# Kernel optimization log

Hardware: AMD Instinct MI355X
Metric: run time of the kernel (lower is better)

## Reference

```python
import jax, jax.numpy as jnp
import numpy as np
from jax.scipy.linalg import expm

DIM = 128
BF = 2          # branching_factor
H = 8           # num_heads
MAX_DEPTH = 12
PAD = BF + 1    # padding value used by pad_sequence in the torch module
N = 256         # number of positions


def setup_inputs() -> dict:
    key = jax.random.key(0)
    k1, k2 = jax.random.split(key)
    # raw _primitives parameter (the torch init applies softmax+cumsum to rand;
    # any values work for the math -- only the skew-hermitian part matters)
    prim = jax.random.uniform(k1, (BF * H + 1, DIM, DIM), dtype=jnp.float32)
    positions = jax.random.randint(k2, (N,), 0, BF ** MAX_DEPTH)  # node indices, >= 0
    return {"primitives_param": prim, "positions": positions}


def _path_words(positions):
    """Vectorized equivalent of create_paths + pad_sequence.

    For node index n the branch path is built by walking up the tree:
    branch = (n-1) % BF, parent = (n-1) // BF. Digits come out leaf->root,
    so we reverse the valid prefix and right-pad with PAD to MAX_DEPTH.
    """
    d = positions.astype(jnp.int32)
    digs = []
    for _ in range(MAX_DEPTH):
        valid = d > 0
        digs.append(jnp.where(valid, (d - 1) % BF, PAD))
        d = jnp.where(valid, (d - 1) // BF, 0)
    R = jnp.stack(digs, axis=1)            # (N, 12) leaf->root digits
    depth = jnp.sum(R != PAD, axis=1)       # path length per token
    idx = depth[:, None] - 1 - jnp.arange(MAX_DEPTH)[None, :]
    pw = jnp.take_along_axis(R, jnp.clip(idx, 0, MAX_DEPTH - 1), axis=1)
    pw = jnp.where(idx >= 0, pw, PAD)       # (N, 12) root->leaf, PAD-padded
    return pw, depth


def reference(primitives_param, positions):
    pw, depth = _path_words(positions)

    # ---- steps matrix (tree distance), mirrors the no_grad block ----
    pm = pw != PAD                                        # (N, 12)
    mask = pm[:, None, :] & pm[None, :, :]                # (N, N, 12)
    eq = pw[:, None, :] == pw[None, :, :]
    common = jnp.cumprod(eq.astype(jnp.int32), axis=-1).astype(bool) & mask
    cpl = common.sum(-1)                                  # common prefix length
    steps = depth[:, None] + depth[None, :] - 2 * cpl     # (N, N) int

    # ---- unitary primitives: expm of the skew(-hermitian, real) part ----
    skew = primitives_param - jnp.swapaxes(primitives_param, -1, -2)
    prims = expm(skew)                                    # (BF*H+1, DIM, DIM)
    sos = prims[-1]
    P = prims[:-1].reshape(BF, H, DIM, DIM)

    n_tok = pw.shape[0]
    maps = jnp.broadcast_to(jnp.eye(DIM, dtype=prims.dtype)[None, None],
                            (n_tok, H, DIM, DIM))
    sos_ptr = pw[:, 0] == -1                              # never true for pos>=0, kept for fidelity
    maps = jnp.where(sos_ptr[:, None, None, None], sos[None, None], maps)

    # fused gather-indexed scan over tree depth: instead of BF masked matmuls
    # per depth, gather each token's branch primitive and do one batched matmul.
    for d in range(MAX_DEPTH):
        sel = pw[:, d]                                    # (N,) in {0..BF-1} or PAD
        Pk = P[jnp.clip(sel, 0, BF - 1)]                  # (N, H, DIM, DIM)
        new = jnp.einsum('nhij,nhjk->nhik', maps, Pk)
        maps = jnp.where((sel < BF)[:, None, None, None], new, maps)

    return maps, steps
```

## Files before the change

### kernel.cpp

```cpp
#include <hip/hip_runtime.h>

typedef unsigned short ushort_t;
typedef unsigned int uint_t;
typedef __attribute__((ext_vector_type(8))) short bf16x8;
typedef __attribute__((ext_vector_type(4))) float f32x4;

#define NMAT 16
#define MSZ 16384
#define NTAB 30

__device__ __forceinline__ ushort_t f32_bf16(float f) {
  uint_t u = __builtin_bit_cast(uint_t, f);
  u += 0x7FFFu + ((u >> 16) & 1u);
  return (ushort_t)(u >> 16);
}

__device__ __forceinline__ float bf16_f32(ushort_t b) {
  uint_t u = ((uint_t)b) << 16;
  return __builtin_bit_cast(float, u);
}

__device__ __forceinline__ int swz(int r, int k) {
  return r * 128 + (((k >> 3) ^ (r & 7)) << 3) + (k & 7);
}

__device__ __forceinline__ int tab_off(int L) {
  return (L == 1) ? 0 : (L == 2) ? 2 : (L == 3) ? 6 : 14;
}

__device__ __forceinline__ void mm_frag(const ushort_t* U, const ushort_t* V,
                                        int r0, int c0, int quad, int l16,
                                        f32x4 (&acc)[4][4]) {
#pragma unroll
  for (int rt = 0; rt < 4; rt++)
#pragma unroll
    for (int ct = 0; ct < 4; ct++) {
      f32x4 z = {0.f, 0.f, 0.f, 0.f};
      acc[rt][ct] = z;
    }
#pragma unroll
  for (int kt = 0; kt < 4; kt++) {
    int k = kt * 32 + quad * 8;
    bf16x8 a[4], b[4];
#pragma unroll
    for (int rt = 0; rt < 4; rt++) a[rt] = *(const bf16x8*)(&U[swz(r0 + rt * 16 + l16, k)]);
#pragma unroll
    for (int ct = 0; ct < 4; ct++) b[ct] = *(const bf16x8*)(&V[swz(c0 + ct * 16 + l16, k)]);
#pragma unroll
    for (int rt = 0; rt < 4; rt++)
#pragma unroll
      for (int ct = 0; ct < 4; ct++)
        acc[rt][ct] = __builtin_amdgcn_mfma_f32_16x16x32_bf16(a[rt], b[ct], acc[rt][ct], 0, 0, 0);
  }
}

__device__ __forceinline__ void store_T(ushort_t* dst, const f32x4 (&acc)[4][4],
                                        int r0, int c0, int quad, int l16,
                                        float scale, float cdiag) {
#pragma unroll
  for (int rt = 0; rt < 4; rt++)
#pragma unroll
    for (int ct = 0; ct < 4; ct++) {
      int dr = r0 + rt * 16 + quad * 4, dc = c0 + ct * 16 + l16;
      float v[4];
#pragma unroll
      for (int i = 0; i < 4; i++) {
        v[i] = scale * acc[rt][ct][i];
        if (dr + i == dc) v[i] += cdiag;
      }
      uint2 pk;
      pk.x = (uint_t)f32_bf16(v[0]) | ((uint_t)f32_bf16(v[1]) << 16);
      pk.y = (uint_t)f32_bf16(v[2]) | ((uint_t)f32_bf16(v[3]) << 16);
      *(uint2*)(&dst[swz(dc, dr)]) = pk;
    }
}

__device__ __forceinline__ void set_ident(ushort_t* dst, int t, float c) {
  ushort_t cb = f32_bf16(c);
  for (int i = 0; i < 64; i++) {
    int e = i * 256 + t;
    int r = e >> 7, k = e & 127;
    dst[swz(r, k)] = (r == k) ? cb : (ushort_t)0;
  }
}

__global__ __launch_bounds__(256, 1) void expm1_kernel(const float* __restrict__ prim,
                                                       ushort_t* __restrict__ wsCS) {
  __shared__ ushort_t __align__(16) bufA[MSZ];
  __shared__ ushort_t __align__(16) bufB[MSZ];
  int kmat = blockIdx.x >> 1, which = blockIdx.x & 1;
  int t = threadIdx.x, wave = t >> 6, lane = t & 63;
  int quad = lane >> 4, l16 = lane & 15;
  int r0 = (wave >> 1) * 64, c0 = (wave & 1) * 64;
  const float* p = prim + kmat * MSZ;

  for (int i = 0; i < 64; i++) {
    int e = i * 256 + t;
    int r = e >> 7, c = e & 127;
    bufA[swz(r, c)] = f32_bf16((p[r * 128 + c] - p[c * 128 + r]) * 0.125f);
  }
  __syncthreads();

  f32x4 acc[4][4];
  mm_frag(bufA, bufA, r0, c0, quad, l16, acc);
  __syncthreads();
  store_T(bufB, acc, r0, c0, quad, l16, -1.f, 0.f);
  __syncthreads();

  uint2 yv[4][4];
#pragma unroll
  for (int rt = 0; rt < 4; rt++)
#pragma unroll
    for (int ct = 0; ct < 4; ct++) {
      int dr = r0 + rt * 16 + quad * 4, dc = c0 + ct * 16 + l16;
      yv[rt][ct] = *(const uint2*)(&bufB[swz(dc, dr)]);
    }

  mm_frag(bufB, bufB, r0, c0, quad, l16, acc);
  __syncthreads();
  store_T(bufB, acc, r0, c0, quad, l16, 1.f, 0.f);

  float coef[9];
  if (which == 0) {
    coef[0] = 1.f; coef[1] = 1.f / 2; coef[2] = 1.f / 24; coef[3] = 1.f / 720;
    coef[4] = 1.f / 40320; coef[5] = 1.f / 3628800.f; coef[6] = 1.f / 479001600.f;
    coef[7] = 1.f / 87178291200.f; coef[8] = 1.f / 20922789888000.f;
  } else {
    coef[0] = 1.f; coef[1] = 1.f / 6; coef[2] = 1.f / 120; coef[3] = 1.f / 5040;
    coef[4] = 1.f / 362880.f; coef[5] = 1.f / 39916800.f; coef[6] = 1.f / 6227020800.f;
    coef[7] = 1.f / 1307674368000.f; coef[8] = 1.f / 355687428096000.f;
  }

  set_ident(bufA, t, coef[8]);
  __syncthreads();

#pragma unroll
  for (int k = 3; k >= 0; k--) {
    mm_frag(bufB, bufA, r0, c0, quad, l16, acc);
    __syncthreads();
    float cd = coef[2 * k], cy = coef[2 * k + 1];
#pragma unroll
    for (int rt = 0; rt < 4; rt++)
#pragma unroll
      for (int ct = 0; ct < 4; ct++) {
        int dr = r0 + rt * 16 + quad * 4, dc = c0 + ct * 16 + l16;
        uint2 yp = yv[rt][ct];
        float y[4] = {bf16_f32((ushort_t)(yp.x & 0xffff)), bf16_f32((ushort_t)(yp.x >> 16)),
                      bf16_f32((ushort_t)(yp.y & 0xffff)), bf16_f32((ushort_t)(yp.y >> 16))};
        float v[4];
#pragma unroll
        for (int i = 0; i < 4; i++) {
          v[i] = acc[rt][ct][i] + cy * y[i];
          if (dr + i == dc) v[i] += cd;
        }
        uint2 pk;
        pk.x = (uint_t)f32_bf16(v[0]) | ((uint_t)f32_bf16(v[1]) << 16);
        pk.y = (uint_t)f32_bf16(v[2]) | ((uint_t)f32_bf16(v[3]) << 16);
        *(uint2*)(&bufA[swz(dc, dr)]) = pk;
      }
    __syncthreads();
  }
  ushort_t* dst = wsCS + (size_t)(which * NMAT + kmat) * MSZ;
  for (int i = 0; i < 8; i++) {
    int e = (i * 256 + t) * 8;
    int r = e >> 7, k = e & 127;
    *(uint4*)(dst + e) = *(const uint4*)(&bufA[swz(r, k)]);
  }
}

__global__ __launch_bounds__(256, 1) void expm2_kernel(
    const float* __restrict__ prim, const ushort_t* __restrict__ wsCS,
    ushort_t* __restrict__ TN, ushort_t* __restrict__ TT) {
  __shared__ ushort_t __align__(16) bufA[MSZ];
  __shared__ ushort_t __align__(16) bufB[MSZ];
  int kmat = blockIdx.x;
  int t = threadIdx.x, wave = t >> 6, lane = t & 63;
  int quad = lane >> 4, l16 = lane & 15;
  int r0 = (wave >> 1) * 64, c0 = (wave & 1) * 64;
  const float* p = prim + kmat * MSZ;
  const ushort_t* Cg = wsCS + (size_t)kmat * MSZ;
  const ushort_t* Sg = wsCS + (size_t)(NMAT + kmat) * MSZ;

  for (int i = 0; i < 64; i++) {
    int e = i * 256 + t;
    int r = e >> 7, c = e & 127;
    bufA[swz(r, c)] = f32_bf16((p[r * 128 + c] - p[c * 128 + r]) * 0.125f);
  }
  for (int i = 0; i < 8; i++) {
    int e = (i * 256 + t) * 8;
    int r = e >> 7, k = e & 127;
    *(uint4*)(&bufB[swz(r, k)]) = *(const uint4*)(Sg + e);
  }
  __syncthreads();

  f32x4 acc[4][4];
  mm_frag(bufA, bufB, r0, c0, quad, l16, acc);
  __syncthreads();
#pragma unroll
  for (int rt = 0; rt < 4; rt++)
#pragma unroll
    for (int ct = 0; ct < 4; ct++) {
      int dr = r0 + rt * 16 + quad * 4, dc = c0 + ct * 16 + l16;
      uint2 cp = *(const uint2*)(Cg + dc * 128 + dr);
      float cf[4] = {bf16_f32((ushort_t)(cp.x & 0xffff)), bf16_f32((ushort_t)(cp.x >> 16)),
                     bf16_f32((ushort_t)(cp.y & 0xffff)), bf16_f32((ushort_t)(cp.y >> 16))};
      uint2 en, et;
      en.x = (uint_t)f32_bf16(cf[0] - acc[rt][ct][0]) | ((uint_t)f32_bf16(cf[1] - acc[rt][ct][1]) << 16);
      en.y = (uint_t)f32_bf16(cf[2] - acc[rt][ct][2]) | ((uint_t)f32_bf16(cf[3] - acc[rt][ct][3]) << 16);
      et.x = (uint_t)f32_bf16(cf[0] + acc[rt][ct][0]) | ((uint_t)f32_bf16(cf[1] + acc[rt][ct][1]) << 16);
      et.y = (uint_t)f32_bf16(cf[2] + acc[rt][ct][2]) | ((uint_t)f32_bf16(cf[3] + acc[rt][ct][3]) << 16);
      *(uint2*)(&bufA[swz(dc, dr)]) = en;
      *(uint2*)(&bufB[swz(dc, dr)]) = et;
    }
  __syncthreads();

#pragma unroll 1
  for (int sq = 0; sq < 3; sq++) {
    mm_frag(bufA, bufB, r0, c0, quad, l16, acc);
    __syncthreads();
#pragma unroll
    for (int rt = 0; rt < 4; rt++)
#pragma unroll
      for (int ct = 0; ct < 4; ct++) {
        int dr = r0 + rt * 16 + quad * 4, dc = c0 + ct * 16 + l16;
        uint2 pk;
        pk.x = (uint_t)f32_bf16(acc[rt][ct][0]) | ((uint_t)f32_bf16(acc[rt][ct][1]) << 16);
        pk.y = (uint_t)f32_bf16(acc[rt][ct][2]) | ((uint_t)f32_bf16(acc[rt][ct][3]) << 16);
        *(uint2*)(&bufB[swz(dc, dr)]) = pk;
#pragma unroll
        for (int i = 0; i < 4; i++) bufA[swz(dr + i, dc)] = f32_bf16(acc[rt][ct][i]);
      }
    __syncthreads();
  }
  for (int i = 0; i < 8; i++) {
    int e = (i * 256 + t) * 8;
    int r = e >> 7, k = e & 127;
    *(uint4*)(TN + (size_t)kmat * MSZ + e) = *(const uint4*)(&bufA[swz(r, k)]);
    *(uint4*)(TT + (size_t)kmat * MSZ + e) = *(const uint4*)(&bufB[swz(r, k)]);
  }
}

__global__ __launch_bounds__(256) void table_kernel(ushort_t* __restrict__ TN,
                                                    ushort_t* __restrict__ TT, int mode) {
  int bx = blockIdx.x;
  int eA, eB, eO, h;
  if (mode == 0) {
    int c = bx >> 3; h = bx & 7;
    eA = c >> 1; eB = c & 1; eO = 2 + c;
  } else {
    if (bx < 64) {
      int c = bx >> 3; h = bx & 7;
      eA = 2 + (c >> 1); eB = c & 1; eO = 6 + c;
    } else {
      int c = (bx - 64) >> 3; h = (bx - 64) & 7;
      eA = 2 + (c >> 2); eB = 2 + (c & 3); eO = 14 + c;
    }
  }
  int t = threadIdx.x, wave = t >> 6, lane = t & 63;
  int quad = lane >> 4, l16 = lane & 15;
  int r0 = (wave >> 1) * 64, c0 = (wave & 1) * 64;
  const ushort_t* A = TN + ((size_t)eA * 8 + h) * MSZ;
  const ushort_t* B = TT + ((size_t)eB * 8 + h) * MSZ;
  ushort_t* oN = TN + ((size_t)eO * 8 + h) * MSZ;
  ushort_t* oT = TT + ((size_t)eO * 8 + h) * MSZ;

  bf16x8 a[4][4], b[4][4];
#pragma unroll
  for (int kt = 0; kt < 4; kt++) {
#pragma unroll
    for (int rt = 0; rt < 4; rt++)
      a[kt][rt] = *(const bf16x8*)(A + (r0 + rt * 16 + l16) * 128 + kt * 32 + quad * 8);
#pragma unroll
    for (int ct = 0; ct < 4; ct++)
      b[kt][ct] = *(const bf16x8*)(B + (c0 + ct * 16 + l16) * 128 + kt * 32 + quad * 8);
  }
  f32x4 acc[4][4];
#pragma unroll
  for (int rt = 0; rt < 4; rt++)
#pragma unroll
    for (int ct = 0; ct < 4; ct++) {
      f32x4 z = {0.f, 0.f, 0.f, 0.f};
      acc[rt][ct] = z;
    }
#pragma unroll
  for (int kt = 0; kt < 4; kt++)
#pragma unroll
    for (int rt = 0; rt < 4; rt++)
#pragma unroll
      for (int ct = 0; ct < 4; ct++)
        acc[rt][ct] = __builtin_amdgcn_mfma_f32_16x16x32_bf16(a[kt][rt], b[kt][ct], acc[rt][ct], 0, 0, 0);
#pragma unroll
  for (int rt = 0; rt < 4; rt++)
#pragma unroll
    for (int ct = 0; ct < 4; ct++) {
      int dr = r0 + rt * 16 + quad * 4, dc = c0 + ct * 16 + l16;
      uint2 pk;
      pk.x = (uint_t)f32_bf16(acc[rt][ct][0]) | ((uint_t)f32_bf16(acc[rt][ct][1]) << 16);
      pk.y = (uint_t)f32_bf16(acc[rt][ct][2]) | ((uint_t)f32_bf16(acc[rt][ct][3]) << 16);
      *(uint2*)(oT + dc * 128 + dr) = pk;
#pragma unroll
      for (int i = 0; i < 4; i++) oN[(dr + i) * 128 + dc] = f32_bf16(acc[rt][ct][i]);
    }
}

__global__ void steps_kernel(const int* __restrict__ pos, float* __restrict__ os, int N) {
  int i = blockIdx.x, j = threadIdx.x;
  int mi = pos[i] + 1, mj = pos[j] + 1;
  int di = 31 - __builtin_clz((unsigned)mi);
  int dj = 31 - __builtin_clz((unsigned)mj);
  int tt = di < dj ? di : dj;
  unsigned x = (unsigned)((mi >> (di - tt)) ^ (mj >> (dj - tt)));
  int cpl = tt - (x ? (32 - __builtin_clz(x)) : 0);
  os[i * N + j] = (float)(di + dj - 2 * cpl);
}

__global__ __launch_bounds__(256, 2) void maps_kernel(
    const ushort_t* __restrict__ TN, const ushort_t* __restrict__ TT,
    const int* __restrict__ positions, float* __restrict__ out) {
  __shared__ ushort_t __align__(16) Mb[2][MSZ];
  int bx = blockIdx.x;
  int n = bx >> 3, h = bx & 7;
  int t = threadIdx.x, wave = t >> 6, lane = t & 63;
  int quad = lane >> 4, l16 = lane & 15;
  int m = positions[n] + 1;
  int depth = 31 - __builtin_clz((unsigned)m);
  float* ob = out + (size_t)(n * 8 + h) * MSZ;

  if (depth == 0) {
    for (int i = 0; i < 64; i++) {
      int e = i * 256 + t;
      int r = e >> 7, k = e & 127;
      ob[e] = (r == k) ? 1.0f : 0.0f;
    }
    return;
  }
  if (depth <= 4) {
    int c = m & ((1 << depth) - 1);
    const ushort_t* src = TN + ((size_t)(tab_off(depth) + c) * 8 + h) * MSZ;
    for (int i = 0; i < 8; i++) {
      int e = (i * 256 + t) * 8;
      bf16x8 v = *(const bf16x8*)(src + e);
      f32x4 lo = {bf16_f32((ushort_t)v[0]), bf16_f32((ushort_t)v[1]),
                  bf16_f32((ushort_t)v[2]), bf16_f32((ushort_t)v[3])};
      f32x4 hi = {bf16_f32((ushort_t)v[4]), bf16_f32((ushort_t)v[5]),
                  bf16_f32((ushort_t)v[6]), bf16_f32((ushort_t)v[7])};
      *(f32x4*)(ob + e) = lo;
      *(f32x4*)(ob + e + 4) = hi;
    }
    return;
  }

  int K = (depth + 3) >> 2;
  int L0 = depth - 4 * (K - 1);
  int c0v = (m >> (depth - L0)) & ((1 << L0) - 1);
  const ushort_t* src0 = TN + ((size_t)(tab_off(L0) + c0v) * 8 + h) * MSZ;
  bool two = (K == 3);
  int c1 = (m >> (4 * (K - 2))) & 15;
  int c2 = m & 15;
  const ushort_t* Ap1 = TT + ((size_t)(14 + c1) * 8 + h) * MSZ;
  const ushort_t* Ap2 = TT + ((size_t)(14 + c2) * 8 + h) * MSZ;

  int r0 = (wave >> 1) * 64, c0 = (wave & 1) * 64;
#pragma unroll
  for (int i = 0; i < 8; i++) {
    int e = (i * 256 + t) * 8;
    int r = e >> 7, k = e & 127;
    *(uint4*)(&Mb[0][swz(r, k)]) = *(const uint4*)(src0 + e);
  }
  bf16x8 a1[4][4];
#pragma unroll
  for (int kt = 0; kt < 4; kt++)
#pragma unroll
    for (int rt = 0; rt < 4; rt++)
      a1[kt][rt] = *(const bf16x8*)(Ap1 + (r0 + rt * 16 + l16) * 128 + kt * 32 + quad * 8);
  __syncthreads();

  f32x4 acc[4][4];
#pragma unroll
  for (int rt = 0; rt < 4; rt++)
#pragma unroll
    for (int ct = 0; ct < 4; ct++) {
      f32x4 z = {0.f, 0.f, 0.f, 0.f};
      acc[rt][ct] = z;
    }
#pragma unroll
  for (int kt = 0; kt < 4; kt++) {
    int k = kt * 32 + quad * 8;
    bf16x8 b[4];
#pragma unroll
    for (int ct = 0; ct < 4; ct++) b[ct] = *(const bf16x8*)(&Mb[0][swz(c0 + ct * 16 + l16, k)]);
#pragma unroll
    for (int rt = 0; rt < 4; rt++)
#pragma unroll
      for (int ct = 0; ct < 4; ct++)
        acc[rt][ct] = __builtin_amdgcn_mfma_f32_16x16x32_bf16(a1[kt][rt], b[ct], acc[rt][ct], 0, 0, 0);
  }

  if (two) {
    bf16x8 a2[4][4];
#pragma unroll
    for (int kt = 0; kt < 4; kt++)
#pragma unroll
      for (int rt = 0; rt < 4; rt++)
        a2[kt][rt] = *(const bf16x8*)(Ap2 + (r0 + rt * 16 + l16) * 128 + kt * 32 + quad * 8);
#pragma unroll
    for (int rt = 0; rt < 4; rt++)
#pragma unroll
      for (int ct = 0; ct < 4; ct++) {
        int dr = r0 + rt * 16 + quad * 4;
        int dc = c0 + ct * 16 + l16;
        uint2 pk;
        pk.x = (uint_t)f32_bf16(acc[rt][ct][0]) | ((uint_t)f32_bf16(acc[rt][ct][1]) << 16);
        pk.y = (uint_t)f32_bf16(acc[rt][ct][2]) | ((uint_t)f32_bf16(acc[rt][ct][3]) << 16);
        *(uint2*)(&Mb[1][swz(dc, dr)]) = pk;
      }
    __syncthreads();

#pragma unroll
    for (int rt = 0; rt < 4; rt++)
#pragma unroll
      for (int ct = 0; ct < 4; ct++) {
        f32x4 z = {0.f, 0.f, 0.f, 0.f};
        acc[rt][ct] = z;
      }
#pragma unroll
    for (int kt = 0; kt < 4; kt++) {
      int k = kt * 32 + quad * 8;
      bf16x8 b[4];
#pragma unroll
      for (int ct = 0; ct < 4; ct++) b[ct] = *(const bf16x8*)(&Mb[1][swz(c0 + ct * 16 + l16, k)]);
#pragma unroll
      for (int rt = 0; rt < 4; rt++)
#pragma unroll
        for (int ct = 0; ct < 4; ct++)
          acc[rt][ct] = __builtin_amdgcn_mfma_f32_16x16x32_bf16(a2[kt][rt], b[ct], acc[rt][ct], 0, 0, 0);
    }
  }

#pragma unroll
  for (int rt = 0; rt < 4; rt++)
#pragma unroll
    for (int ct = 0; ct < 4; ct++) {
      int dr = r0 + rt * 16 + quad * 4;
      int dc = c0 + ct * 16 + l16;
      *(f32x4*)(ob + dc * 128 + dr) = acc[rt][ct];
    }
}

extern "C" void kernel_launch(void* const* d_in, const int* in_sizes, int n_in,
                              void* d_out, int out_size, void* d_ws, size_t ws_size,
                              hipStream_t stream) {
  const float* prim = (const float*)d_in[0];
  const int* positions = (const int*)d_in[1];
  int N = in_sizes[1];
  float* out = (float*)d_out;

  ushort_t* wsCS = (ushort_t*)d_ws;
  ushort_t* TN = wsCS + (size_t)2 * NMAT * MSZ;
  ushort_t* TT = TN + (size_t)NTAB * 8 * MSZ;

  steps_kernel<<<N, N, 0, stream>>>(positions, out + (size_t)N * 8 * MSZ, N);
  expm1_kernel<<<2 * NMAT, 256, 0, stream>>>(prim, wsCS);
  expm2_kernel<<<NMAT, 256, 0, stream>>>(prim, wsCS, TN, TT);
  table_kernel<<<32, 256, 0, stream>>>(TN, TT, 0);
  table_kernel<<<192, 256, 0, stream>>>(TN, TT, 1);
  maps_kernel<<<N * 8, 256, 0, stream>>>(TN, TT, positions, out);
}
```

Baseline: 221.4 us.

## Fuse steps into expm1, merge table kernels, stage transpose through LDS

Folds the steps-matrix computation into extra blocks of the first expm kernel, which removes one launch. The two table-building launches become a single launch in which depth-3 and depth-4 entries are recomputed from the base entries through chained in-block matmuls in LDS, removing the launch dependency between them. The skew-part construction now stages the fp32 matrix in swizzled shared memory so the transposed read no longer hits global memory uncoalesced. The cost is redundant matmul work in the table blocks and an added bf16 rounding for intermediate products.

Result: slower. 231.8 us (+4.7%).

```diff
diff --git a/kernel.cpp b/kernel.cpp
--- a/kernel.cpp
+++ b/kernel.cpp
@@ -46,6 +46,58 @@
     for (int rt = 0; rt < 4; rt++) a[rt] = *(const bf16x8*)(&U[swz(r0 + rt * 16 + l16, k)]);
 #pragma unroll
     for (int ct = 0; ct < 4; ct++) b[ct] = *(const bf16x8*)(&V[swz(c0 + ct * 16 + l16, k)]);
+#pragma unroll
+    for (int rt = 0; rt < 4; rt++)
+#pragma unroll
+      for (int ct = 0; ct < 4; ct++)
+        acc[rt][ct] = __builtin_amdgcn_mfma_f32_16x16x32_bf16(a[rt], b[ct], acc[rt][ct], 0, 0, 0);
+  }
+}
+
+__device__ __forceinline__ void mm_gg(const ushort_t* gU, const ushort_t* gV,
+                                      int r0, int c0, int quad, int l16,
+                                      f32x4 (&acc)[4][4]) {
+#pragma unroll
+  for (int rt = 0; rt < 4; rt++)
+#pragma unroll
+    for (int ct = 0; ct < 4; ct++) {
+      f32x4 z = {0.f, 0.f, 0.f, 0.f};
+      acc[rt][ct] = z;
+    }
+#pragma unroll
+  for (int kt = 0; kt < 4; kt++) {
+    int k = kt * 32 + quad * 8;
+    bf16x8 a[4], b[4];
+#pragma unroll
+    for (int rt = 0; rt < 4; rt++) a[rt] = *(const bf16x8*)(gU + (r0 + rt * 16 + l16) * 128 + k);
+#pragma unroll
+    for (int ct = 0; ct < 4; ct++) b[ct] = *(const bf16x8*)(gV + (c0 + ct * 16 + l16) * 128 + k);
+#pragma unroll
+    for (int rt = 0; rt < 4; rt++)
+#pragma unroll
+      for (int ct = 0; ct < 4; ct++)
+        acc[rt][ct] = __builtin_amdgcn_mfma_f32_16x16x32_bf16(a[rt], b[ct], acc[rt][ct], 0, 0, 0);
+  }
+}
+
+__device__ __forceinline__ void mm_lg(const ushort_t* lU, const ushort_t* gV,
+                                      int r0, int c0, int quad, int l16,
+                                      f32x4 (&acc)[4][4]) {
+#pragma unroll
+  for (int rt = 0; rt < 4; rt++)
+#pragma unroll
+    for (int ct = 0; ct < 4; ct++) {
+      f32x4 z = {0.f, 0.f, 0.f, 0.f};
+      acc[rt][ct] = z;
+    }
+#pragma unroll
+  for (int kt = 0; kt < 4; kt++) {
+    int k = kt * 32 + quad * 8;
+    bf16x8 a[4], b[4];
+#pragma unroll
+    for (int rt = 0; rt < 4; rt++) a[rt] = *(const bf16x8*)(&lU[swz(r0 + rt * 16 + l16, k)]);
+#pragma unroll
+    for (int ct = 0; ct < 4; ct++) b[ct] = *(const bf16x8*)(gV + (c0 + ct * 16 + l16) * 128 + k);
 #pragma unroll
     for (int rt = 0; rt < 4; rt++)
 #pragma unroll
@@ -84,12 +136,30 @@
   }
 }
 
-__global__ __launch_bounds__(256, 1) void expm1_kernel(const float* __restrict__ prim,
-                                                       ushort_t* __restrict__ wsCS) {
-  __shared__ ushort_t __align__(16) bufA[MSZ];
-  __shared__ ushort_t __align__(16) bufB[MSZ];
-  int kmat = blockIdx.x >> 1, which = blockIdx.x & 1;
-  int t = threadIdx.x, wave = t >> 6, lane = t & 63;
+__global__ __launch_bounds__(256, 1) void expm1_kernel(
+    const float* __restrict__ prim, ushort_t* __restrict__ wsCS,
+    const int* __restrict__ pos, float* __restrict__ os, int N) {
+  int bx = blockIdx.x;
+  int t = threadIdx.x;
+  if (bx >= 32) {
+    int i = bx - 32, j = t;
+    int mi = pos[i] + 1, mj = pos[j] + 1;
+    int di = 31 - __builtin_clz((unsigned)mi);
+    int dj = 31 - __builtin_clz((unsigned)mj);
+    int tt = di < dj ? di : dj;
+    unsigned x = (unsigned)((mi >> (di - tt)) ^ (mj >> (dj - tt)));
+    int cpl = tt - (x ? (32 - __builtin_clz(x)) : 0);
+    os[i * N + j] = (float)(di + dj - 2 * cpl);
+    return;
+  }
+
+  __shared__ ushort_t __align__(16) smem[2 * MSZ];
+  ushort_t* bufA = smem;
+  ushort_t* bufB = smem + MSZ;
+  float* pf = (float*)smem;
+
+  int kmat = bx >> 1, which = bx & 1;
+  int wave = t >> 6, lane = t & 63;
   int quad = lane >> 4, l16 = lane & 15;
   int r0 = (wave >> 1) * 64, c0 = (wave & 1) * 64;
   const float* p = prim + kmat * MSZ;
@@ -97,7 +167,24 @@
   for (int i = 0; i < 64; i++) {
     int e = i * 256 + t;
     int r = e >> 7, c = e & 127;
-    bufA[swz(r, c)] = f32_bf16((p[r * 128 + c] - p[c * 128 + r]) * 0.125f);
+    pf[r * 128 + (c ^ (r & 31))] = p[e];
+  }
+  __syncthreads();
+  ushort_t xr[64];
+#pragma unroll
+  for (int i = 0; i < 64; i++) {
+    int e = i * 256 + t;
+    int r = e >> 7, c = e & 127;
+    float a = pf[r * 128 + (c ^ (r & 31))];
+    float b = pf[c * 128 + (r ^ (c & 31))];
+    xr[i] = f32_bf16((a - b) * 0.125f);
+  }
+  __syncthreads();
+#pragma unroll
+  for (int i = 0; i < 64; i++) {
+    int e = i * 256 + t;
+    int r = e >> 7, c = e & 127;
+    bufA[swz(r, c)] = xr[i];
   }
   __syncthreads();
 
@@ -171,8 +258,10 @@
 __global__ __launch_bounds__(256, 1) void expm2_kernel(
     const float* __restrict__ prim, const ushort_t* __restrict__ wsCS,
     ushort_t* __restrict__ TN, ushort_t* __restrict__ TT) {
-  __shared__ ushort_t __align__(16) bufA[MSZ];
-  __shared__ ushort_t __align__(16) bufB[MSZ];
+  __shared__ ushort_t __align__(16) smem[2 * MSZ];
+  ushort_t* bufA = smem;
+  ushort_t* bufB = smem + MSZ;
+  float* pf = (float*)smem;
   int kmat = blockIdx.x;
   int t = threadIdx.x, wave = t >> 6, lane = t & 63;
   int quad = lane >> 4, l16 = lane & 15;
@@ -184,7 +273,24 @@
   for (int i = 0; i < 64; i++) {
     int e = i * 256 + t;
     int r = e >> 7, c = e & 127;
-    bufA[swz(r, c)] = f32_bf16((p[r * 128 + c] - p[c * 128 + r]) * 0.125f);
+    pf[r * 128 + (c ^ (r & 31))] = p[e];
+  }
+  __syncthreads();
+  ushort_t xr[64];
+#pragma unroll
+  for (int i = 0; i < 64; i++) {
+    int e = i * 256 + t;
+    int r = e >> 7, c = e & 127;
+    float a = pf[r * 128 + (c ^ (r & 31))];
+    float b = pf[c * 128 + (r ^ (c & 31))];
+    xr[i] = f32_bf16((a - b) * 0.125f);
+  }
+  __syncthreads();
+#pragma unroll
+  for (int i = 0; i < 64; i++) {
+    int e = i * 256 + t;
+    int r = e >> 7, c = e & 127;
+    bufA[swz(r, c)] = xr[i];
   }
   for (int i = 0; i < 8; i++) {
     int e = (i * 256 + t) * 8;
@@ -241,54 +347,45 @@
 }
 
 __global__ __launch_bounds__(256) void table_kernel(ushort_t* __restrict__ TN,
-                                                    ushort_t* __restrict__ TT, int mode) {
+                                                    ushort_t* __restrict__ TT) {
+  __shared__ ushort_t __align__(16) LA[MSZ];
+  __shared__ ushort_t __align__(16) LB[MSZ];
   int bx = blockIdx.x;
-  int eA, eB, eO, h;
-  if (mode == 0) {
-    int c = bx >> 3; h = bx & 7;
-    eA = c >> 1; eB = c & 1; eO = 2 + c;
-  } else {
-    if (bx < 64) {
-      int c = bx >> 3; h = bx & 7;
-      eA = 2 + (c >> 1); eB = c & 1; eO = 6 + c;
-    } else {
-      int c = (bx - 64) >> 3; h = (bx - 64) & 7;
-      eA = 2 + (c >> 2); eB = 2 + (c & 3); eO = 14 + c;
-    }
-  }
+  int idx = bx >> 3, h = bx & 7;
   int t = threadIdx.x, wave = t >> 6, lane = t & 63;
   int quad = lane >> 4, l16 = lane & 15;
   int r0 = (wave >> 1) * 64, c0 = (wave & 1) * 64;
-  const ushort_t* A = TN + ((size_t)eA * 8 + h) * MSZ;
-  const ushort_t* B = TT + ((size_t)eB * 8 + h) * MSZ;
+  f32x4 acc[4][4];
+  int eO;
+  (void)t;
+
+  if (idx < 4) {
+    int c = idx; eO = 2 + c;
+    mm_gg(TN + ((size_t)(c >> 1) * 8 + h) * MSZ,
+          TT + ((size_t)(c & 1) * 8 + h) * MSZ, r0, c0, quad, l16, acc);
+  } else if (idx < 12) {
+    int c = idx - 4; eO = 6 + c;
+    int a = c >> 2, b = (c >> 1) & 1, last = c & 1;
+    mm_gg(TT + ((size_t)b * 8 + h) * MSZ,
+          TN + ((size_t)a * 8 + h) * MSZ, r0, c0, quad, l16, acc);
+    store_T(LA, acc, r0, c0, quad, l16, 1.f, 0.f);
+    __syncthreads();
+    mm_lg(LA, TT + ((size_t)last * 8 + h) * MSZ, r0, c0, quad, l16, acc);
+  } else {
+    int c = idx - 12; eO = 14 + c;
+    int a = c >> 3, b = (c >> 2) & 1, cc = (c >> 1) & 1, d = c & 1;
+    mm_gg(TT + ((size_t)b * 8 + h) * MSZ,
+          TN + ((size_t)a * 8 + h) * MSZ, r0, c0, quad, l16, acc);
+    store_T(LA, acc, r0, c0, quad, l16, 1.f, 0.f);
+    mm_gg(TN + ((size_t)cc * 8 + h) * MSZ,
+          TT + ((size_t)d * 8 + h) * MSZ, r0, c0, quad, l16, acc);
+    store_T(LB, acc, r0, c0, quad, l16, 1.f, 0.f);
+    __syncthreads();
+    mm_frag(LA, LB, r0, c0, quad, l16, acc);
+  }
+
   ushort_t* oN = TN + ((size_t)eO * 8 + h) * MSZ;
   ushort_t* oT = TT + ((size_t)eO * 8 + h) * MSZ;
-
-  bf16x8 a[4][4], b[4][4];
-#pragma unroll
-  for (int kt = 0; kt < 4; kt++) {
-#pragma unroll
-    for (int rt = 0; rt < 4; rt++)
-      a[kt][rt] = *(const bf16x8*)(A + (r0 + rt * 16 + l16) * 128 + kt * 32 + quad * 8);
-#pragma unroll
-    for (int ct = 0; ct < 4; ct++)
-      b[kt][ct] = *(const bf16x8*)(B + (c0 + ct * 16 + l16) * 128 + kt * 32 + quad * 8);
-  }
-  f32x4 acc[4][4];
-#pragma unroll
-  for (int rt = 0; rt < 4; rt++)
-#pragma unroll
-    for (int ct = 0; ct < 4; ct++) {
-      f32x4 z = {0.f, 0.f, 0.f, 0.f};
-      acc[rt][ct] = z;
-    }
-#pragma unroll
-  for (int kt = 0; kt < 4; kt++)
-#pragma unroll
-    for (int rt = 0; rt < 4; rt++)
-#pragma unroll
-      for (int ct = 0; ct < 4; ct++)
-        acc[rt][ct] = __builtin_amdgcn_mfma_f32_16x16x32_bf16(a[kt][rt], b[kt][ct], acc[rt][ct], 0, 0, 0);
 #pragma unroll
   for (int rt = 0; rt < 4; rt++)
 #pragma unroll
@@ -301,17 +398,6 @@
 #pragma unroll
       for (int i = 0; i < 4; i++) oN[(dr + i) * 128 + dc] = f32_bf16(acc[rt][ct][i]);
     }
-}
-
-__global__ void steps_kernel(const int* __restrict__ pos, float* __restrict__ os, int N) {
-  int i = blockIdx.x, j = threadIdx.x;
-  int mi = pos[i] + 1, mj = pos[j] + 1;
-  int di = 31 - __builtin_clz((unsigned)mi);
-  int dj = 31 - __builtin_clz((unsigned)mj);
-  int tt = di < dj ? di : dj;
-  unsigned x = (unsigned)((mi >> (di - tt)) ^ (mj >> (dj - tt)));
-  int cpl = tt - (x ? (32 - __builtin_clz(x)) : 0);
-  os[i * N + j] = (float)(di + dj - 2 * cpl);
 }
 
 __global__ __launch_bounds__(256, 2) void maps_kernel(
@@ -459,10 +545,9 @@
   ushort_t* TN = wsCS + (size_t)2 * NMAT * MSZ;
   ushort_t* TT = TN + (size_t)NTAB * 8 * MSZ;
 
-  steps_kernel<<<N, N, 0, stream>>>(positions, out + (size_t)N * 8 * MSZ, N);
-  expm1_kernel<<<2 * NMAT, 256, 0, stream>>>(prim, wsCS);
+  float* steps_out = out + (size_t)N * 8 * MSZ;
+  expm1_kernel<<<32 + N, 256, 0, stream>>>(prim, wsCS, positions, steps_out, N);
   expm2_kernel<<<NMAT, 256, 0, stream>>>(prim, wsCS, TN, TT);
-  table_kernel<<<32, 256, 0, stream>>>(TN, TT, 0);
-  table_kernel<<<192, 256, 0, stream>>>(TN, TT, 1);
+  table_kernel<<<224, 256, 0, stream>>>(TN, TT);
   maps_kernel<<<N * 8, 256, 0, stream>>>(TN, TT, positions, out);
 }
```
